# Performance work log

Measured on AMD Instinct MI355X. Metric: run time of the kernel, lower is better.

Reference implementation:

```python
import jax, jax.numpy as jnp
import numpy as np

NUM_CLASSES = 32768
FEAT_DIM = 512
BATCH = 1024


def setup_inputs() -> dict:
    key = jax.random.key(0)
    k1, k2, k3 = jax.random.split(key, 3)
    x = jax.random.normal(k1, (BATCH, FEAT_DIM), dtype=jnp.float32)
    labels = jax.random.randint(k2, (BATCH,), 0, NUM_CLASSES, dtype=jnp.int64)
    centers = jax.random.normal(k3, (NUM_CLASSES, FEAT_DIM), dtype=jnp.float32)
    return {"x": x, "labels": labels, "centers": centers}


def reference(x, labels, centers):
    # Original computes full cdist(x, centers)**2 / 2 and masks to the
    # label-matched column; mathematically identical to gathering each
    # sample's own center and taking half the squared L2 distance.
    c = centers[labels]                       # [B, D] gather
    diff = x - c                              # [B, D]
    per_sample = 0.5 * jnp.sum(diff * diff, axis=1)  # [B]
    return jnp.mean(per_sample)               # reduction='mean'
```

## Files before the change

kernel.cpp:

```cpp
#include <hip/hip_runtime.h>

#define BATCH 1024
#define FEAT_DIM 512

__global__ __launch_bounds__(256) void cl_partial(
    const float* __restrict__ x,
    const int* __restrict__ labels,
    const float* __restrict__ centers,
    float* __restrict__ ws)
{
    const int wave = threadIdx.x >> 6;
    const int lane = threadIdx.x & 63;
    const int b    = blockIdx.x * 4 + wave;

    const int label = labels[b];

    const float4* __restrict__ xr =
        reinterpret_cast<const float4*>(x + (size_t)b * FEAT_DIM);
    const float4* __restrict__ cr =
        reinterpret_cast<const float4*>(centers + (size_t)label * FEAT_DIM);

    const float4 a0 = xr[lane];
    const float4 a1 = xr[lane + 64];
    const float4 c0 = cr[lane];
    const float4 c1 = cr[lane + 64];

    float d0 = a0.x - c0.x, d1 = a0.y - c0.y, d2 = a0.z - c0.z, d3 = a0.w - c0.w;
    float d4 = a1.x - c1.x, d5 = a1.y - c1.y, d6 = a1.z - c1.z, d7 = a1.w - c1.w;

    float s = d0 * d0 + d1 * d1 + d2 * d2 + d3 * d3
            + d4 * d4 + d5 * d5 + d6 * d6 + d7 * d7;

    #pragma unroll
    for (int off = 32; off > 0; off >>= 1)
        s += __shfl_down(s, off, 64);

    if (lane == 0) ws[b] = s;
}

__global__ __launch_bounds__(64) void cl_final(
    const float* __restrict__ ws,
    float* __restrict__ out)
{
    const int lane = threadIdx.x;
    const float4* __restrict__ w = reinterpret_cast<const float4*>(ws);

    const float4 v0 = w[lane];
    const float4 v1 = w[lane + 64];
    const float4 v2 = w[lane + 128];
    const float4 v3 = w[lane + 192];

    float s = v0.x + v0.y + v0.z + v0.w
            + v1.x + v1.y + v1.z + v1.w
            + v2.x + v2.y + v2.z + v2.w
            + v3.x + v3.y + v3.z + v3.w;

    #pragma unroll
    for (int off = 32; off > 0; off >>= 1)
        s += __shfl_down(s, off, 64);

    if (lane == 0) out[0] = s * (0.5f / (float)BATCH);
}

extern "C" void kernel_launch(void* const* d_in, const int* in_sizes, int n_in,
                              void* d_out, int out_size, void* d_ws, size_t ws_size,
                              hipStream_t stream) {
    const float* x       = (const float*)d_in[0];
    const int*   labels  = (const int*)d_in[1];
    const float* centers = (const float*)d_in[2];
    float*       out     = (float*)d_out;
    float*       ws      = (float*)d_ws;

    cl_partial<<<BATCH / 4, 256, 0, stream>>>(x, labels, centers, ws);
    cl_final<<<1, 64, 0, stream>>>(ws, out);
}
```

Before: 11.25 us.

## Fuse partial and final reduction into one cooperative kernel with grid sync

```diff
diff --git a/kernel.cpp b/kernel.cpp
--- a/kernel.cpp
+++ b/kernel.cpp
@@ -1,13 +1,17 @@
 #include <hip/hip_runtime.h>
+#include <hip/hip_cooperative_groups.h>
+
+namespace cg = cooperative_groups;
 
 #define BATCH 1024
 #define FEAT_DIM 512
 
-__global__ __launch_bounds__(256) void cl_partial(
+__global__ __launch_bounds__(256) void cl_coop(
     const float* __restrict__ x,
     const int* __restrict__ labels,
     const float* __restrict__ centers,
-    float* __restrict__ ws)
+    float* __restrict__ ws,
+    float* __restrict__ out)
 {
     const int wave = threadIdx.x >> 6;
     const int lane = threadIdx.x & 63;
@@ -25,8 +29,10 @@
     const float4 c0 = cr[lane];
     const float4 c1 = cr[lane + 64];
 
-    float d0 = a0.x - c0.x, d1 = a0.y - c0.y, d2 = a0.z - c0.z, d3 = a0.w - c0.w;
-    float d4 = a1.x - c1.x, d5 = a1.y - c1.y, d6 = a1.z - c1.z, d7 = a1.w - c1.w;
+    const float d0 = a0.x - c0.x, d1 = a0.y - c0.y;
+    const float d2 = a0.z - c0.z, d3 = a0.w - c0.w;
+    const float d4 = a1.x - c1.x, d5 = a1.y - c1.y;
+    const float d6 = a1.z - c1.z, d7 = a1.w - c1.w;
 
     float s = d0 * d0 + d1 * d1 + d2 * d2 + d3 * d3
             + d4 * d4 + d5 * d5 + d6 * d6 + d7 * d7;
@@ -35,31 +41,23 @@
     for (int off = 32; off > 0; off >>= 1)
         s += __shfl_down(s, off, 64);
 
-    if (lane == 0) ws[b] = s;
-}
+    __shared__ float wsum[4];
+    if (lane == 0) wsum[wave] = s;
+    __syncthreads();
 
-__global__ __launch_bounds__(64) void cl_final(
-    const float* __restrict__ ws,
-    float* __restrict__ out)
-{
-    const int lane = threadIdx.x;
-    const float4* __restrict__ w = reinterpret_cast<const float4*>(ws);
+    if (threadIdx.x == 0)
+        ws[blockIdx.x] = wsum[0] + wsum[1] + wsum[2] + wsum[3];
 
-    const float4 v0 = w[lane];
-    const float4 v1 = w[lane + 64];
-    const float4 v2 = w[lane + 128];
-    const float4 v3 = w[lane + 192];
+    cg::this_grid().sync();
 
-    float s = v0.x + v0.y + v0.z + v0.w
-            + v1.x + v1.y + v1.z + v1.w
-            + v2.x + v2.y + v2.z + v2.w
-            + v3.x + v3.y + v3.z + v3.w;
-
-    #pragma unroll
-    for (int off = 32; off > 0; off >>= 1)
-        s += __shfl_down(s, off, 64);
-
-    if (lane == 0) out[0] = s * (0.5f / (float)BATCH);
+    if (blockIdx.x == 0 && threadIdx.x < 64) {
+        const int l = threadIdx.x;
+        float t = ws[l] + ws[l + 64] + ws[l + 128] + ws[l + 192];
+        #pragma unroll
+        for (int off = 32; off > 0; off >>= 1)
+            t += __shfl_down(t, off, 64);
+        if (l == 0) out[0] = t * (0.5f / (float)BATCH);
+    }
 }
 
 extern "C" void kernel_launch(void* const* d_in, const int* in_sizes, int n_in,
@@ -71,6 +69,8 @@
     float*       out     = (float*)d_out;
     float*       ws      = (float*)d_ws;
 
-    cl_partial<<<BATCH / 4, 256, 0, stream>>>(x, labels, centers, ws);
-    cl_final<<<1, 64, 0, stream>>>(ws, out);
+    void* args[] = {(void*)&x, (void*)&labels, (void*)&centers,
+                    (void*)&ws, (void*)&out};
+    hipLaunchCooperativeKernel((const void*)cl_coop, dim3(256), dim3(256),
+                               args, 0, stream);
 }
```

After: 38.06 us. 3.38x slower.
